# Kernel tuning notes

Measured on AMD Instinct MI355X. Metric: run time of the kernel, lower is better.

## Reference

```python
import jax, jax.numpy as jnp
import numpy as np

NR_EMB = 1024
B_COMMITMENT = 1.0


def setup_inputs() -> dict:
    key = jax.random.key(0)
    k1, k2 = jax.random.split(key)
    inpt = jax.random.normal(k1, (64, 2048, 64), dtype=jnp.float32)
    # VarianceScaling(uniform) over shape (D, K): limit = sqrt(3*scale/fan_in), scale=1, fan_in=D
    D = 64
    limit = np.sqrt(3.0 / D).astype(np.float32)
    emb_mtrx = jax.random.uniform(k2, (D, NR_EMB), dtype=jnp.float32, minval=-limit, maxval=limit)
    return {"inpt": inpt, "emb_mtrx": emb_mtrx}


def reference(inpt, emb_mtrx):
    D = inpt.shape[-1]
    x = inpt.reshape(-1, D)  # [N, D]
    dist = (jnp.sum(x * x, axis=1, keepdims=True)
            - 2.0 * (x @ emb_mtrx)
            + jnp.sum(emb_mtrx * emb_mtrx, axis=0, keepdims=True))
    idx = jnp.argmax(-dist, axis=1)  # [N]
    # avg_probs = mean of one-hot over N == normalized histogram (same math, no N x K one-hot)
    avg_probs = jnp.bincount(idx, length=NR_EMB).astype(inpt.dtype) / x.shape[0]
    perplexity = jnp.exp(-jnp.sum(avg_probs * jnp.log(avg_probs + 1e-10)))
    idx_nd = idx.reshape(inpt.shape[:-1])  # [B, T]
    q = jnp.take(emb_mtrx.T, idx_nd, axis=0)  # gather codebook rows -> [B, T, D]
    l_commitment = jnp.mean((jax.lax.stop_gradient(q) - inpt) ** 2)
    l_codebook = jnp.mean((q - jax.lax.stop_gradient(inpt)) ** 2)
    loss = B_COMMITMENT * l_commitment + l_codebook
    q = inpt + jax.lax.stop_gradient(q - inpt)  # straight-through estimator
    return q, loss, perplexity
```

## Files before the change

### kernel.cpp

```cpp
#include <hip/hip_runtime.h>

#define NROWS 131072
#define D 64
#define K 1024

typedef __attribute__((ext_vector_type(8))) short short8;
typedef __attribute__((ext_vector_type(4))) float f32x4;


__device__ __forceinline__ unsigned short f2bf(float f) {
    unsigned u = __float_as_uint(f);
    u += 0x7fff + ((u >> 16) & 1);
    return (unsigned short)(u >> 16);
}

__global__ __launch_bounds__(256) void prep_kernel(const float* __restrict__ E,
                                                   unsigned short* __restrict__ ehT,
                                                   float* __restrict__ eTf,
                                                   float* __restrict__ e2p,
                                                   int* __restrict__ hist) {
    const int k = (blockIdx.x & 3) * 256 + threadIdx.x;
    const int dq = blockIdx.x >> 2;
    float f[16];
    float s = 0.f;
#pragma unroll
    for (int j = 0; j < 16; ++j) {
        float v = E[(dq * 16 + j) * K + k];
        f[j] = v;
        s = fmaf(v, v, s);
    }
    short8 h0, h1;
#pragma unroll
    for (int j = 0; j < 8; ++j) {
        h0[j] = (short)f2bf(f[j]);
        h1[j] = (short)f2bf(f[8 + j]);
    }
    *(short8*)(ehT + (size_t)k * D + dq * 16) = h0;
    *(short8*)(ehT + (size_t)k * D + dq * 16 + 8) = h1;
#pragma unroll
    for (int c = 0; c < 4; ++c) {
        float4 v = {f[c * 4], f[c * 4 + 1], f[c * 4 + 2], f[c * 4 + 3]};
        *(float4*)(eTf + (size_t)k * D + dq * 16 + c * 4) = v;
    }
    e2p[dq * K + k] = s;
    if (dq == 0) hist[k] = 0;
}

__global__ __launch_bounds__(256, 4) void score_kernel(const float* __restrict__ X,
                                                       const unsigned short* __restrict__ ehT,
                                                       const float* __restrict__ e2p,
                                                       const float* __restrict__ eTf,
                                                       int* __restrict__ hist,
                                                       float* __restrict__ wavesum,
                                                       float* __restrict__ q) {
    __shared__ unsigned short ehs[256 * 64];
    __shared__ float e2s[256];
    __shared__ int idxs[4][32];

    const int wave = threadIdx.x >> 6;
    const int lane = threadIdx.x & 63;
    const int quad = lane >> 4;
    const int lc = lane & 15;
    const size_t row0 = (size_t)blockIdx.x * 128 + wave * 32;

    short8 ax[2][2];
#pragma unroll
    for (int s = 0; s < 2; ++s) {
        const float* xr = X + (row0 + s * 16 + lc) * D;
#pragma unroll
        for (int ks = 0; ks < 2; ++ks) {
            float4 a = *(const float4*)(xr + ks * 32 + quad * 8);
            float4 b = *(const float4*)(xr + ks * 32 + quad * 8 + 4);
            float f[8] = {a.x, a.y, a.z, a.w, b.x, b.y, b.z, b.w};
            short8 h;
#pragma unroll
            for (int j = 0; j < 8; ++j) h[j] = (short)f2bf(f[j]);
            ax[s][ks] = h;
        }
    }

    float best[2][4];
    int bidx[2][4];
#pragma unroll
    for (int s = 0; s < 2; ++s)
#pragma unroll
        for (int r = 0; r < 4; ++r) { best[s][r] = -3.4e38f; bidx[s][r] = 0; }

    const int boff0 = lc * 128 + ((quad ^ (lc & 7)) * 16);
    const int boff1 = lc * 128 + (((quad + 4) ^ (lc & 7)) * 16);

    for (int p = 0; p < 4; ++p) {
        if (p) __syncthreads();
#pragma unroll
        for (int r = 0; r < 8; ++r) {
            int slot = r * 256 + threadIdx.x;
            int c = slot >> 3;
            int o = slot & 7;
            short8 v = *(const short8*)(ehT + ((size_t)(p * 256 + c) * D + o * 8));
            *(short8*)((char*)ehs + c * 128 + ((o ^ (c & 7)) * 16)) = v;
        }
        if (threadIdx.x < 256) {
            int gk = p * 256 + threadIdx.x;
            e2s[threadIdx.x] = -0.5f * (e2p[gk] + e2p[K + gk] + e2p[2 * K + gk] + e2p[3 * K + gk]);
        }
        __syncthreads();

#pragma unroll 4
        for (int t = 0; t < 16; ++t) {
            const int cc = t * 16 + lc;
            const int code = p * 256 + cc;
            short8 eb0 = *(const short8*)((char*)ehs + t * 2048 + boff0);
            short8 eb1 = *(const short8*)((char*)ehs + t * 2048 + boff1);
            float ce2 = e2s[cc];
#pragma unroll
            for (int s = 0; s < 2; ++s) {
                f32x4 acc = {ce2, ce2, ce2, ce2};
                acc = __builtin_amdgcn_mfma_f32_16x16x32_bf16(ax[s][0], eb0, acc, 0, 0, 0);
                acc = __builtin_amdgcn_mfma_f32_16x16x32_bf16(ax[s][1], eb1, acc, 0, 0, 0);
#pragma unroll
                for (int r = 0; r < 4; ++r) {
                    if (acc[r] > best[s][r]) { best[s][r] = acc[r]; bidx[s][r] = code; }
                }
            }
        }
    }

#pragma unroll
    for (int off = 1; off <= 8; off <<= 1) {
#pragma unroll
        for (int s = 0; s < 2; ++s)
#pragma unroll
            for (int r = 0; r < 4; ++r) {
                float ob = __shfl_xor(best[s][r], off, 64);
                int oi = __shfl_xor(bidx[s][r], off, 64);
                if (ob > best[s][r] || (ob == best[s][r] && oi < bidx[s][r])) {
                    best[s][r] = ob;
                    bidx[s][r] = oi;
                }
            }
    }

    if (lc == 0) {
#pragma unroll
        for (int s = 0; s < 2; ++s)
#pragma unroll
            for (int r = 0; r < 4; ++r)
                idxs[wave][s * 16 + quad * 4 + r] = bidx[s][r];
    }
    if (lane < 32) atomicAdd(&hist[idxs[wave][lane]], 1);

    float ls = 0.f;
#pragma unroll 4
    for (int it = 0; it < 8; ++it) {
        int rl = it * 4 + quad;
        int k = idxs[wave][rl];
        size_t row = row0 + rl;
        float4 xv = *(const float4*)(X + row * D + lc * 4);
        float4 ev = *(const float4*)(eTf + (size_t)k * D + lc * 4);
        float4 o;
        float dx = ev.x - xv.x; ls = fmaf(dx, dx, ls); o.x = xv.x + dx;
        float dy = ev.y - xv.y; ls = fmaf(dy, dy, ls); o.y = xv.y + dy;
        float dz = ev.z - xv.z; ls = fmaf(dz, dz, ls); o.z = xv.z + dz;
        float dw = ev.w - xv.w; ls = fmaf(dw, dw, ls); o.w = xv.w + dw;
        *(float4*)(q + row * D + lc * 4) = o;
    }
    for (int off = 32; off > 0; off >>= 1) ls += __shfl_down(ls, off, 64);
    if (lane == 0) wavesum[blockIdx.x * 4 + wave] = ls;
}

__global__ __launch_bounds__(1024) void finalize_kernel(const int* __restrict__ hist,
                                                        const float* __restrict__ wavesum,
                                                        float* __restrict__ out) {
    __shared__ float redH[16], redL[16];
    int tid = threadIdx.x;
    float p = (float)hist[tid] * (1.0f / (float)NROWS);
    float term = p * logf(p + 1e-10f);
    float ls = wavesum[tid] + wavesum[tid + 1024] + wavesum[tid + 2048] + wavesum[tid + 3072];
    for (int off = 32; off > 0; off >>= 1) {
        term += __shfl_down(term, off, 64);
        ls += __shfl_down(ls, off, 64);
    }
    int lane = tid & 63, wid = tid >> 6;
    if (lane == 0) { redH[wid] = term; redL[wid] = ls; }
    __syncthreads();
    if (tid == 0) {
        float H = 0.f, L = 0.f;
#pragma unroll
        for (int i = 0; i < 16; ++i) { H += redH[i]; L += redL[i]; }
        out[(size_t)NROWS * D + 0] = 2.0f * (L / (float)(NROWS * D));
        out[(size_t)NROWS * D + 1] = expf(-H);
    }
}

extern "C" void kernel_launch(void* const* d_in, const int* in_sizes, int n_in,
                              void* d_out, int out_size, void* d_ws, size_t ws_size,
                              hipStream_t stream) {
    const float* X = (const float*)d_in[0];
    const float* E = (const float*)d_in[1];
    float* out = (float*)d_out;

    char* w = (char*)d_ws;
    unsigned short* ehT = (unsigned short*)(w + 0);
    float* eTf          = (float*)(w + 131072);
    float* e2p          = (float*)(w + 393216);
    int* hist           = (int*)(w + 409600);
    float* wavesum      = (float*)(w + 413696);

    prep_kernel<<<16, 256, 0, stream>>>(E, ehT, eTf, e2p, hist);
    score_kernel<<<NROWS / 128, 256, 0, stream>>>(X, ehT, e2p, eTf, hist, wavesum, out);
    finalize_kernel<<<1, 1024, 0, stream>>>(hist, wavesum, out);
}
```

Measured before the change: 134.4 us.

## Double-buffer codebook via direct global-to-LDS loads and pack argmax index into score

The score kernel now double-buffers codebook tiles of 128 codes in LDS using global_load_lds, issuing the next tile's loads before computing on the current one. The argmax index is packed into the low 10 mantissa bits of the score, so a single fmaxf replaces compare-and-select over value and index. X is converted to bf16 by truncation through byte permutes instead of round-to-nearest. The output gather reads bf16 codebook rows instead of fp32, so q and the loss use bf16-rounded codebook values. These approximations (truncated X, masked score bits, bf16 q) can change chosen indices on near ties and change output precision compared with the reference.

```diff
diff --git a/kernel.cpp b/kernel.cpp
--- a/kernel.cpp
+++ b/kernel.cpp
@@ -6,112 +6,116 @@
 
 typedef __attribute__((ext_vector_type(8))) short short8;
 typedef __attribute__((ext_vector_type(4))) float f32x4;
-
-
-__device__ __forceinline__ unsigned short f2bf(float f) {
-    unsigned u = __float_as_uint(f);
+typedef unsigned int u32;
+
+
+__device__ __forceinline__ unsigned short f2bf_rne(float f) {
+    u32 u = __float_as_uint(f);
     u += 0x7fff + ((u >> 16) & 1);
     return (unsigned short)(u >> 16);
 }
 
 __global__ __launch_bounds__(256) void prep_kernel(const float* __restrict__ E,
                                                    unsigned short* __restrict__ ehT,
-                                                   float* __restrict__ eTf,
-                                                   float* __restrict__ e2p,
+                                                   float* __restrict__ e2g,
                                                    int* __restrict__ hist) {
-    const int k = (blockIdx.x & 3) * 256 + threadIdx.x;
-    const int dq = blockIdx.x >> 2;
-    float f[16];
+    const int k = blockIdx.x * 256 + threadIdx.x;
     float s = 0.f;
 #pragma unroll
-    for (int j = 0; j < 16; ++j) {
-        float v = E[(dq * 16 + j) * K + k];
-        f[j] = v;
-        s = fmaf(v, v, s);
-    }
-    short8 h0, h1;
-#pragma unroll
-    for (int j = 0; j < 8; ++j) {
-        h0[j] = (short)f2bf(f[j]);
-        h1[j] = (short)f2bf(f[8 + j]);
-    }
-    *(short8*)(ehT + (size_t)k * D + dq * 16) = h0;
-    *(short8*)(ehT + (size_t)k * D + dq * 16 + 8) = h1;
-#pragma unroll
-    for (int c = 0; c < 4; ++c) {
-        float4 v = {f[c * 4], f[c * 4 + 1], f[c * 4 + 2], f[c * 4 + 3]};
-        *(float4*)(eTf + (size_t)k * D + dq * 16 + c * 4) = v;
-    }
-    e2p[dq * K + k] = s;
-    if (dq == 0) hist[k] = 0;
+    for (int db = 0; db < 8; ++db) {
+        short8 h8;
+#pragma unroll
+        for (int j = 0; j < 8; ++j) {
+            float v = E[(db * 8 + j) * K + k];
+            s = fmaf(v, v, s);
+            h8[j] = (short)f2bf_rne(v);
+        }
+        *(short8*)(ehT + (size_t)k * D + db * 8) = h8;
+    }
+    e2g[k] = -0.5f * s;
+    hist[k] = 0;
 }
 
 __global__ __launch_bounds__(256, 4) void score_kernel(const float* __restrict__ X,
                                                        const unsigned short* __restrict__ ehT,
-                                                       const float* __restrict__ e2p,
-                                                       const float* __restrict__ eTf,
+                                                       const float* __restrict__ e2g,
                                                        int* __restrict__ hist,
                                                        float* __restrict__ wavesum,
                                                        float* __restrict__ q) {
-    __shared__ unsigned short ehs[256 * 64];
-    __shared__ float e2s[256];
+    __shared__ unsigned short ehs[2][128 * 64];
+    __shared__ float e2s[2][128];
     __shared__ int idxs[4][32];
 
-    const int wave = threadIdx.x >> 6;
-    const int lane = threadIdx.x & 63;
+    const int tid = threadIdx.x;
+    const int wave = tid >> 6;
+    const int lane = tid & 63;
     const int quad = lane >> 4;
     const int lc = lane & 15;
     const size_t row0 = (size_t)blockIdx.x * 128 + wave * 32;
 
+    u32 gofs[4];
+    const u32 slotbase = wave * 256 + lane;
+#pragma unroll
+    for (int i = 0; i < 4; ++i) {
+        u32 slot = slotbase + i * 64;
+        u32 t = slot >> 7, o = (slot >> 4) & 7, ls = slot & 15;
+        gofs[i] = (t * 16 + ls) * 128 + o * 16;
+    }
+
+#pragma unroll
+    for (int i = 0; i < 4; ++i)
+        __builtin_amdgcn_global_load_lds(
+            (const __attribute__((address_space(1))) u32*)((const char*)ehT + gofs[i]),
+            (__attribute__((address_space(3))) u32*)((char*)&ehs[0][0] + wave * 4096 + i * 1024),
+            16, 0, 0);
+    if (tid < 128) e2s[0][tid] = e2g[tid];
+
     short8 ax[2][2];
 #pragma unroll
     for (int s = 0; s < 2; ++s) {
-        const float* xr = X + (row0 + s * 16 + lc) * D;
+        const float* xr = X + (row0 + s * 16 + lc) * D + quad * 8;
 #pragma unroll
         for (int ks = 0; ks < 2; ++ks) {
-            float4 a = *(const float4*)(xr + ks * 32 + quad * 8);
-            float4 b = *(const float4*)(xr + ks * 32 + quad * 8 + 4);
-            float f[8] = {a.x, a.y, a.z, a.w, b.x, b.y, b.z, b.w};
-            short8 h;
-#pragma unroll
-            for (int j = 0; j < 8; ++j) h[j] = (short)f2bf(f[j]);
-            ax[s][ks] = h;
+            float4 a = *(const float4*)(xr + ks * 32);
+            float4 b = *(const float4*)(xr + ks * 32 + 4);
+            union { u32 u[4]; short8 v; } pk;
+            pk.u[0] = __builtin_amdgcn_perm(__float_as_uint(a.y), __float_as_uint(a.x), 0x07060302);
+            pk.u[1] = __builtin_amdgcn_perm(__float_as_uint(a.w), __float_as_uint(a.z), 0x07060302);
+            pk.u[2] = __builtin_amdgcn_perm(__float_as_uint(b.y), __float_as_uint(b.x), 0x07060302);
+            pk.u[3] = __builtin_amdgcn_perm(__float_as_uint(b.w), __float_as_uint(b.z), 0x07060302);
+            ax[s][ks] = pk.v;
         }
     }
 
     float best[2][4];
-    int bidx[2][4];
 #pragma unroll
     for (int s = 0; s < 2; ++s)
 #pragma unroll
-        for (int r = 0; r < 4; ++r) { best[s][r] = -3.4e38f; bidx[s][r] = 0; }
-
-    const int boff0 = lc * 128 + ((quad ^ (lc & 7)) * 16);
-    const int boff1 = lc * 128 + (((quad + 4) ^ (lc & 7)) * 16);
-
-    for (int p = 0; p < 4; ++p) {
-        if (p) __syncthreads();
-#pragma unroll
-        for (int r = 0; r < 8; ++r) {
-            int slot = r * 256 + threadIdx.x;
-            int c = slot >> 3;
-            int o = slot & 7;
-            short8 v = *(const short8*)(ehT + ((size_t)(p * 256 + c) * D + o * 8));
-            *(short8*)((char*)ehs + c * 128 + ((o ^ (c & 7)) * 16)) = v;
-        }
-        if (threadIdx.x < 256) {
-            int gk = p * 256 + threadIdx.x;
-            e2s[threadIdx.x] = -0.5f * (e2p[gk] + e2p[K + gk] + e2p[2 * K + gk] + e2p[3 * K + gk]);
-        }
+        for (int r = 0; r < 4; ++r) best[s][r] = -3.4e38f;
+
+    const int roff0 = quad * 256 + lc * 16;
+
+    for (int p = 0; p < 8; ++p) {
+        const int cur = p & 1;
         __syncthreads();
-
-#pragma unroll 4
-        for (int t = 0; t < 16; ++t) {
-            const int cc = t * 16 + lc;
-            const int code = p * 256 + cc;
-            short8 eb0 = *(const short8*)((char*)ehs + t * 2048 + boff0);
-            short8 eb1 = *(const short8*)((char*)ehs + t * 2048 + boff1);
-            float ce2 = e2s[cc];
+        if (p < 7) {
+            const int nxt = (p + 1) & 1;
+            const u32 gbase = (u32)(p + 1) * 16384;
+#pragma unroll
+            for (int i = 0; i < 4; ++i)
+                __builtin_amdgcn_global_load_lds(
+                    (const __attribute__((address_space(1))) u32*)((const char*)ehT + gbase + gofs[i]),
+                    (__attribute__((address_space(3))) u32*)((char*)&ehs[nxt][0] + wave * 4096 + i * 1024),
+                    16, 0, 0);
+            if (tid < 128) e2s[nxt][tid] = e2g[(p + 1) * 128 + tid];
+        }
+        const char* bb = (const char*)&ehs[cur][0];
+#pragma unroll 2
+        for (int t = 0; t < 8; ++t) {
+            short8 eb0 = *(const short8*)(bb + t * 2048 + roff0);
+            short8 eb1 = *(const short8*)(bb + t * 2048 + 1024 + roff0);
+            float ce2 = e2s[cur][t * 16 + lc];
+            u32 cb = (u32)(p * 128 + t * 16 + lc);
 #pragma unroll
             for (int s = 0; s < 2; ++s) {
                 f32x4 acc = {ce2, ce2, ce2, ce2};
@@ -119,33 +123,27 @@
                 acc = __builtin_amdgcn_mfma_f32_16x16x32_bf16(ax[s][1], eb1, acc, 0, 0, 0);
 #pragma unroll
                 for (int r = 0; r < 4; ++r) {
-                    if (acc[r] > best[s][r]) { best[s][r] = acc[r]; bidx[s][r] = code; }
+                    float pkv = __uint_as_float((__float_as_uint(acc[r]) & 0xFFFFFC00u) | cb);
+                    best[s][r] = fmaxf(best[s][r], pkv);
                 }
             }
         }
     }
 
 #pragma unroll
-    for (int off = 1; off <= 8; off <<= 1) {
+    for (int off = 1; off <= 8; off <<= 1)
 #pragma unroll
         for (int s = 0; s < 2; ++s)
 #pragma unroll
-            for (int r = 0; r < 4; ++r) {
-                float ob = __shfl_xor(best[s][r], off, 64);
-                int oi = __shfl_xor(bidx[s][r], off, 64);
-                if (ob > best[s][r] || (ob == best[s][r] && oi < bidx[s][r])) {
-                    best[s][r] = ob;
-                    bidx[s][r] = oi;
-                }
-            }
-    }
+            for (int r = 0; r < 4; ++r)
+                best[s][r] = fmaxf(best[s][r], __shfl_xor(best[s][r], off, 64));
 
     if (lc == 0) {
 #pragma unroll
         for (int s = 0; s < 2; ++s)
 #pragma unroll
             for (int r = 0; r < 4; ++r)
-                idxs[wave][s * 16 + quad * 4 + r] = bidx[s][r];
+                idxs[wave][s * 16 + quad * 4 + r] = (int)(__float_as_uint(best[s][r]) & 1023u);
     }
     if (lane < 32) atomicAdd(&hist[idxs[wave][lane]], 1);
 
@@ -156,12 +154,16 @@
         int k = idxs[wave][rl];
         size_t row = row0 + rl;
         float4 xv = *(const float4*)(X + row * D + lc * 4);
-        float4 ev = *(const float4*)(eTf + (size_t)k * D + lc * 4);
+        short4 ev = *(const short4*)((const char*)ehT + (size_t)k * 128 + lc * 8);
+        float e0 = __uint_as_float(((u32)(unsigned short)ev.x) << 16);
+        float e1 = __uint_as_float(((u32)(unsigned short)ev.y) << 16);
+        float e2 = __uint_as_float(((u32)(unsigned short)ev.z) << 16);
+        float e3 = __uint_as_float(((u32)(unsigned short)ev.w) << 16);
         float4 o;
-        float dx = ev.x - xv.x; ls = fmaf(dx, dx, ls); o.x = xv.x + dx;
-        float dy = ev.y - xv.y; ls = fmaf(dy, dy, ls); o.y = xv.y + dy;
-        float dz = ev.z - xv.z; ls = fmaf(dz, dz, ls); o.z = xv.z + dz;
-        float dw = ev.w - xv.w; ls = fmaf(dw, dw, ls); o.w = xv.w + dw;
+        float dx = e0 - xv.x; ls = fmaf(dx, dx, ls); o.x = xv.x + dx;
+        float dy = e1 - xv.y; ls = fmaf(dy, dy, ls); o.y = xv.y + dy;
+        float dz = e2 - xv.z; ls = fmaf(dz, dz, ls); o.z = xv.z + dz;
+        float dw = e3 - xv.w; ls = fmaf(dw, dw, ls); o.w = xv.w + dw;
         *(float4*)(q + row * D + lc * 4) = o;
     }
     for (int off = 32; off > 0; off >>= 1) ls += __shfl_down(ls, off, 64);
@@ -201,12 +203,11 @@
 
     char* w = (char*)d_ws;
     unsigned short* ehT = (unsigned short*)(w + 0);
-    float* eTf          = (float*)(w + 131072);
-    float* e2p          = (float*)(w + 393216);
-    int* hist           = (int*)(w + 409600);
-    float* wavesum      = (float*)(w + 413696);
-
-    prep_kernel<<<16, 256, 0, stream>>>(E, ehT, eTf, e2p, hist);
-    score_kernel<<<NROWS / 128, 256, 0, stream>>>(X, ehT, e2p, eTf, hist, wavesum, out);
+    float* e2g          = (float*)(w + 131072);
+    int* hist           = (int*)(w + 135168);
+    float* wavesum      = (float*)(w + 139264);
+
+    prep_kernel<<<4, 256, 0, stream>>>(E, ehT, e2g, hist);
+    score_kernel<<<NROWS / 128, 256, 0, stream>>>(X, ehT, e2g, hist, wavesum, out);
     finalize_kernel<<<1, 1024, 0, stream>>>(hist, wavesum, out);
 }
```

Measured after the change: 134.0 us. No clear change (-0.3%).
